# Kernel optimization log

Measured on AMD Instinct MI355X. Metric: run time of the kernel, lower is better.

## Reference

```python
import jax, jax.numpy as jnp
import numpy as np

N = 50000
E = 800000
F_IN = 128
H = 128
C = 16


def _balanced_conv(x, row, col, W, b, num_nodes):
    # x: [N, in] -> linear -> gather(row) * norm -> scatter-add(col) + bias
    x = x @ W  # [N, out]
    deg = jax.ops.segment_sum(jnp.ones(row.shape[0], x.dtype), col,
                              num_segments=num_nodes)  # includes self-loops -> deg >= 1
    dinv = deg ** -0.5
    norm = dinv[row] * dinv[col]  # [E+N]
    msg = norm[:, None] * x[row]  # gather + scale
    out = jax.ops.segment_sum(msg, col, num_segments=num_nodes)  # scatter-add
    return out + b


def setup_inputs() -> dict:
    key = jax.random.key(0)
    ks = jax.random.split(key, 12)
    x = jax.random.normal(ks[0], (N, F_IN), dtype=jnp.float32)
    edge_index = jax.random.randint(ks[1], (2, E), 0, N, dtype=jnp.int64)
    s = 1.0 / np.sqrt(F_IN)
    sh = 1.0 / np.sqrt(H)
    return {
        "x": x,
        "edge_index": edge_index,
        "importance": jnp.ones((F_IN,), jnp.float32),
        "W1": jax.random.uniform(ks[2], (F_IN, H), jnp.float32, -s, s),
        "b1": jnp.zeros((H,), jnp.float32),
        "W2": jax.random.uniform(ks[3], (H, H), jnp.float32, -sh, sh),
        "b2": jnp.zeros((H,), jnp.float32),
        "W3": jax.random.uniform(ks[4], (H, H), jnp.float32, -sh, sh),
        "b3": jnp.zeros((H,), jnp.float32),
        "lw1": jax.random.uniform(ks[5], (H, H), jnp.float32, -sh, sh),
        "lb1": jax.random.uniform(ks[6], (H,), jnp.float32, -sh, sh),
        "lw2": jax.random.uniform(ks[7], (H, C), jnp.float32, -sh, sh),
        "lb2": jax.random.uniform(ks[8], (C,), jnp.float32, -sh, sh),
    }


def reference(x, edge_index, importance, W1, b1, W2, b2, W3, b3, lw1, lb1, lw2, lb2):
    num_nodes = x.shape[0]
    # add self-loops (static shape: E + N)
    loops = jnp.arange(num_nodes, dtype=edge_index.dtype)
    row = jnp.concatenate([edge_index[0], loops])
    col = jnp.concatenate([edge_index[1], loops])

    gelu = lambda t: jax.nn.gelu(t, approximate=False)  # torch F.gelu default = erf

    h = x * importance  # FeatureImportance
    h = gelu(_balanced_conv(h, row, col, W1, b1, num_nodes))
    h = gelu(_balanced_conv(h, row, col, W2, b2, num_nodes))
    h = gelu(_balanced_conv(h, row, col, W3, b3, num_nodes))
    h = gelu(h @ lw1 + lb1)
    return h @ lw2 + lb2  # [N, C]
```

## Files before the change

### kernel.cpp

```cpp
#include <hip/hip_runtime.h>
#include <math.h>

#define NNODES 50000
#define NEDGES 800000
#define FDIM 128
#define NBUCKET 196
#define BCAP 6144
#define ABLK 261
#define EPWA 3072
#define MGRID 782

typedef unsigned short ushortT;
typedef unsigned int uintT;
typedef __attribute__((ext_vector_type(8))) short short8;
typedef __attribute__((ext_vector_type(4))) float floatx4;

__device__ __forceinline__ float gelu_erf(float x){
    return 0.5f * x * (1.0f + erff(x * 0.70710678118654752f));
}
__device__ __forceinline__ float bflo(uintT u){ return __uint_as_float(u << 16); }
__device__ __forceinline__ float bfhi(uintT u){ return __uint_as_float(u & 0xFFFF0000u); }
__device__ __forceinline__ ushortT f2bf(float f){
    uintT u = __float_as_uint(f);
    return (ushortT)((u + 0x7FFFu + ((u >> 16) & 1u)) >> 16);
}
__device__ __forceinline__ void split_bf16(float f, ushortT& hi, ushortT& lo){
    uintT u = __float_as_uint(f);
    hi = (ushortT)(u >> 16);
    float fhi = __uint_as_float(u & 0xFFFF0000u);
    lo = (ushortT)(__float_as_uint(f - fhi) >> 16);
}

__global__ void k_zero(int* __restrict__ gcur){
    if (threadIdx.x < NBUCKET) gcur[threadIdx.x] = 0;
}

__global__ __launch_bounds__(256) void k_bucketA(const int* __restrict__ ei,
                                                 int* __restrict__ gcur,
                                                 uintT* __restrict__ bucket){
    __shared__ int hist[NBUCKET];
    __shared__ int base[NBUCKET];
    int t = threadIdx.x;
    if (t < NBUCKET) hist[t] = 0;
    __syncthreads();
    int e0 = blockIdx.x * EPWA;
    int cr_c[12], cr_r[12];
    #pragma unroll
    for (int p = 0; p < 12; p++){
        int e = e0 + p*256 + t;
        if (e < NEDGES){
            cr_r[p] = ei[e];
            cr_c[p] = ei[NEDGES + e];
            atomicAdd(&hist[cr_c[p] >> 8], 1);
        } else cr_c[p] = -1;
    }
    __syncthreads();
    if (t < NBUCKET){
        base[t] = atomicAdd(&gcur[t], hist[t]);
        hist[t] = 0;
    }
    __syncthreads();
    #pragma unroll
    for (int p = 0; p < 12; p++){
        int c = cr_c[p];
        if (c >= 0){
            int b = c >> 8;
            int lp = atomicAdd(&hist[b], 1);
            bucket[(size_t)b*BCAP + base[b] + lp] = ((uintT)c << 16) | (uintT)cr_r[p];
        }
    }
}

__global__ __launch_bounds__(256) void k_bucketB(const int* __restrict__ gcur,
                                                 const uintT* __restrict__ bucket,
                                                 int* __restrict__ offs,
                                                 float* __restrict__ dinv,
                                                 ushortT* __restrict__ csr2){
    __shared__ int sm[256];
    __shared__ int hist[256];
    __shared__ int lcur[256];
    int b = blockIdx.x;
    int t = threadIdx.x;
    int n0 = b << 8;

    int gv = (t < NBUCKET) ? gcur[t] : 0;
    sm[t] = gv;
    __syncthreads();
    for (int off = 1; off < 256; off <<= 1){
        int tv = (t >= off) ? sm[t-off] : 0;
        __syncthreads();
        sm[t] += tv;
        __syncthreads();
    }
    __shared__ int bbase_s;
    if (t == b) bbase_s = sm[t] - gv;
    hist[t] = 0;
    __syncthreads();
    int bbase = bbase_s;
    int count = gcur[b];
    const uintT* src = bucket + (size_t)b*BCAP;

    for (int i = t; i < count; i += 256)
        atomicAdd(&hist[(src[i] >> 16) & 255], 1);
    __syncthreads();

    int v = hist[t];
    sm[t] = v;
    __syncthreads();
    for (int off = 1; off < 256; off <<= 1){
        int tv = (t >= off) ? sm[t-off] : 0;
        __syncthreads();
        sm[t] += tv;
        __syncthreads();
    }
    int excl = bbase + sm[t] - v;
    int node = n0 + t;
    if (node <= NNODES) offs[node] = excl;
    if (node < NNODES) dinv[node] = rsqrtf((float)(v + 1));
    if (b == NBUCKET-1 && t == 255) offs[NNODES] = NEDGES;
    lcur[t] = excl;
    __syncthreads();

    for (int i = t; i < count; i += 256){
        uintT e = src[i];
        int pos = atomicAdd(&lcur[(e >> 16) & 255], 1);
        csr2[pos] = (ushortT)(e & 0xFFFFu);
    }
}

__global__ __launch_bounds__(256) void k_packW(const float* __restrict__ Wa,
                                               const float* __restrict__ Wb,
                                               const float* __restrict__ Wc,
                                               const float* __restrict__ Wd,
                                               ushortT* __restrict__ Wp){
    int l = blockIdx.x;
    const float* W = (l==0) ? Wa : (l==1) ? Wb : (l==2) ? Wc : Wd;
    ushortT* hiP = Wp + (size_t)l*2*16384;
    ushortT* loP = hiP + 16384;
    for (int idx = threadIdx.x; idx < 16384; idx += 256){
        int k = idx >> 7, n = idx & 127;
        ushortT hi, lo;
        split_bf16(W[idx], hi, lo);
        int kc = k >> 5, quad = (k >> 3) & 3, j = k & 7;
        int nt = n >> 4, lane = (n & 15) + (quad << 4);
        int off = ((kc*8 + nt)*64 + lane)*8 + j;
        hiP[off] = hi;
        loP[off] = lo;
    }
}

template<int OUTMODE>
__global__ __launch_bounds__(256) void k_mfma(const float* __restrict__ A,
                                              const ushortT* __restrict__ Wp,
                                              const float* __restrict__ scale,
                                              const float* __restrict__ dinv,
                                              const float* __restrict__ bias,
                                              void* __restrict__ Yout){
    int t = threadIdx.x;
    int wave = t >> 6, lane = t & 63;
    int r = lane & 15, quad = lane >> 4;
    int m0 = blockIdx.x*64 + wave*16;
    int arow = m0 + r;
    if (arow >= NNODES) arow = NNODES - 1;
    const ushortT* WpLo = Wp + 16384;

    floatx4 acc[8];
    #pragma unroll
    for (int nt = 0; nt < 8; nt++) acc[nt] = (floatx4){0.f,0.f,0.f,0.f};

    #pragma unroll
    for (int kc = 0; kc < 4; kc++){
        int kb = kc*32 + quad*8;
        float4 a0 = *(const float4*)&A[(size_t)arow*FDIM + kb];
        float4 a1 = *(const float4*)&A[(size_t)arow*FDIM + kb + 4];
        if (scale){
            float4 s0 = *(const float4*)&scale[kb];
            float4 s1 = *(const float4*)&scale[kb + 4];
            a0.x*=s0.x; a0.y*=s0.y; a0.z*=s0.z; a0.w*=s0.w;
            a1.x*=s1.x; a1.y*=s1.y; a1.z*=s1.z; a1.w*=s1.w;
        }
        float av[8] = {a0.x, a0.y, a0.z, a0.w, a1.x, a1.y, a1.z, a1.w};
        short8 ahi, alo;
        #pragma unroll
        for (int e = 0; e < 8; e++){
            ushortT h, l;
            split_bf16(av[e], h, l);
            ahi[e] = (short)h;
            alo[e] = (short)l;
        }
        #pragma unroll
        for (int nt = 0; nt < 8; nt++){
            size_t boff = (size_t)(((kc*8 + nt)*64 + lane))*8;
            short8 bhi = *(const short8*)&Wp[boff];
            short8 blo = *(const short8*)&WpLo[boff];
            acc[nt] = __builtin_amdgcn_mfma_f32_16x16x32_bf16(ahi, bhi, acc[nt], 0, 0, 0);
            acc[nt] = __builtin_amdgcn_mfma_f32_16x16x32_bf16(alo, bhi, acc[nt], 0, 0, 0);
            acc[nt] = __builtin_amdgcn_mfma_f32_16x16x32_bf16(ahi, blo, acc[nt], 0, 0, 0);
        }
    }

    int orow0 = m0 + quad*4;
    if (OUTMODE == 1){
        float4 dv = *(const float4*)&dinv[orow0];
        float dva[4] = {dv.x, dv.y, dv.z, dv.w};
        ushortT* Yb = (ushortT*)Yout;
        #pragma unroll
        for (int nt = 0; nt < 8; nt++){
            int n = nt*16 + r;
            int chunk = n >> 5, o = n & 31;
            #pragma unroll
            for (int reg = 0; reg < 4; reg++){
                int orow = orow0 + reg;
                if (orow < NNODES){
                    float v = acc[nt][reg] * dva[reg];
                    Yb[((size_t)chunk*NNODES + orow)*32 + o] = f2bf(v);
                }
            }
        }
    } else {
        float* Yf = (float*)Yout;
        #pragma unroll
        for (int nt = 0; nt < 8; nt++){
            int n = nt*16 + r;
            float bv = bias[n];
            #pragma unroll
            for (int reg = 0; reg < 4; reg++){
                int orow = orow0 + reg;
                if (orow < NNODES){
                    Yf[(size_t)orow*FDIM + n] = gelu_erf(acc[nt][reg] + bv);
                }
            }
        }
    }
}

__global__ __launch_bounds__(256) void k_aggregate(const ushortT* __restrict__ Yt,
                                                   const float* __restrict__ dinv,
                                                   const int* __restrict__ offs,
                                                   const ushortT* __restrict__ csr2,
                                                   const float* __restrict__ bias,
                                                   float* __restrict__ Hout){
    int bid = blockIdx.x;
    int chunk = bid & 3;
    int node = (bid >> 2) * 16 + (threadIdx.x >> 4);
    int lane = threadIdx.x & 15;
    const uintT* Yc = (const uintT*)Yt + (size_t)chunk * NNODES * 16;

    uintT a0 = Yc[node*16 + lane];
    float2 acc;
    acc.x = bflo(a0);
    acc.y = bfhi(a0);
    int e0 = offs[node], e1 = offs[node+1];
    int e = e0;
    for (; e + 3 < e1; e += 4){
        int r0 = csr2[e+0];
        int r1 = csr2[e+1];
        int r2 = csr2[e+2];
        int r3 = csr2[e+3];
        uintT q0 = Yc[r0*16 + lane];
        uintT q1 = Yc[r1*16 + lane];
        uintT q2 = Yc[r2*16 + lane];
        uintT q3 = Yc[r3*16 + lane];
        acc.x += bflo(q0); acc.y += bfhi(q0);
        acc.x += bflo(q1); acc.y += bfhi(q1);
        acc.x += bflo(q2); acc.y += bfhi(q2);
        acc.x += bflo(q3); acc.y += bfhi(q3);
    }
    for (; e < e1; e++){
        int r = csr2[e];
        uintT q = Yc[r*16 + lane];
        acc.x += bflo(q); acc.y += bfhi(q);
    }
    float dc = dinv[node];
    float2 bv = ((const float2*)bias)[chunk*16 + lane];
    acc.x = gelu_erf(fmaf(dc, acc.x, bv.x));
    acc.y = gelu_erf(fmaf(dc, acc.y, bv.y));
    float* dst = &Hout[(size_t)node*FDIM + chunk*32 + lane*2];
    __builtin_nontemporal_store(acc.x, dst);
    __builtin_nontemporal_store(acc.y, dst+1);
}

__global__ __launch_bounds__(256) void k_gemm16(const float* __restrict__ A,
                                                const float* __restrict__ W,
                                                const float* __restrict__ bias,
                                                float* __restrict__ out){
    __shared__ float Hs[16][132];
    __shared__ float Ws2[128][16];
    int row0 = blockIdx.x * 16;
    int t = threadIdx.x;
    #pragma unroll
    for (int p=0;p<8;p++){
        int lin = p*256 + t;
        int r = lin >> 7, c = lin & 127;
        Hs[r][c] = A[(row0+r)*FDIM + c];
    }
    #pragma unroll
    for (int p=0;p<8;p++){
        int lin = p*256 + t;
        Ws2[lin>>4][lin&15] = W[lin];
    }
    __syncthreads();
    int il = t >> 4, j = t & 15;
    float acc = bias[j];
    #pragma unroll
    for (int k=0;k<FDIM;k++) acc = fmaf(Hs[il][k], Ws2[k][j], acc);
    out[(row0+il)*16 + j] = acc;
}

extern "C" void kernel_launch(void* const* d_in, const int* in_sizes, int n_in,
                              void* d_out, int out_size, void* d_ws, size_t ws_size,
                              hipStream_t stream) {
    const float* x    = (const float*)d_in[0];
    const int*   ei   = (const int*)d_in[1];
    const float* imp  = (const float*)d_in[2];
    const float* W1   = (const float*)d_in[3];
    const float* b1   = (const float*)d_in[4];
    const float* W2   = (const float*)d_in[5];
    const float* b2   = (const float*)d_in[6];
    const float* W3   = (const float*)d_in[7];
    const float* b3   = (const float*)d_in[8];
    const float* lw1  = (const float*)d_in[9];
    const float* lb1  = (const float*)d_in[10];
    const float* lw2  = (const float*)d_in[11];
    const float* lb2  = (const float*)d_in[12];
    float* out = (float*)d_out;

    int*   offs   = (int*)d_ws;
    int*   gcur   = (int*)d_ws + 50048;
    float* dinv   = (float*)d_ws + 50304;
    ushortT* csr2 = (ushortT*)((int*)d_ws + 100480);
    uintT* bucket = (uintT*)((int*)d_ws + 500480);
    ushortT* Wp   = (ushortT*)((int*)d_ws + 1704704);
    ushortT* bufYt= (ushortT*)((int*)d_ws + 1770240);
    float* bufY   = (float*)d_ws + 1770240;
    float* bufH   = (float*)d_ws + 8170240;

    dim3 B(256);
    k_packW  <<<4, B, 0, stream>>>(W1, W2, W3, lw1, Wp);
    k_zero   <<<1, B, 0, stream>>>(gcur);
    k_bucketA<<<ABLK, B, 0, stream>>>(ei, gcur, bucket);
    k_bucketB<<<NBUCKET, B, 0, stream>>>(gcur, bucket, offs, dinv, csr2);

    k_mfma<1><<<MGRID, B, 0, stream>>>(x,    Wp + 0*32768, imp,     dinv, nullptr, (void*)bufYt);
    k_aggregate<<<(NNODES/16)*4, B, 0, stream>>>(bufYt, dinv, offs, csr2, b1, bufH);
    k_mfma<1><<<MGRID, B, 0, stream>>>(bufH, Wp + 1*32768, nullptr, dinv, nullptr, (void*)bufYt);
    k_aggregate<<<(NNODES/16)*4, B, 0, stream>>>(bufYt, dinv, offs, csr2, b2, bufH);
    k_mfma<1><<<MGRID, B, 0, stream>>>(bufH, Wp + 2*32768, nullptr, dinv, nullptr, (void*)bufYt);
    k_aggregate<<<(NNODES/16)*4, B, 0, stream>>>(bufYt, dinv, offs, csr2, b3, bufH);

    k_mfma<0><<<MGRID, B, 0, stream>>>(bufH, Wp + 3*32768, nullptr, nullptr, lb1, (void*)bufY);
    k_gemm16<<<NNODES/16, B, 0, stream>>>(bufY, lw2, lb2, out);
}
```

Before: 360.7 us.

## Stage GEMM A tile through LDS, nontemporal bf16 stores, unroll gather by eight

The MFMA GEMM kernel now loads its 64-row A tile into shared memory with coalesced float4 loads, applying the feature scale there, before the per-lane fragment reads. Previously each lane read its row with strided global loads. Its bf16 output stores become nontemporal. The aggregation loop is unrolled from 4 to 8 neighbours with a 2-wide tail, putting more independent gathers in flight at the cost of extra registers and about 33KB of LDS per GEMM block.

```diff
diff --git a/kernel.cpp b/kernel.cpp
--- a/kernel.cpp
+++ b/kernel.cpp
@@ -156,29 +156,40 @@
                                               const float* __restrict__ dinv,
                                               const float* __restrict__ bias,
                                               void* __restrict__ Yout){
+    __shared__ float As[64*132];
     int t = threadIdx.x;
     int wave = t >> 6, lane = t & 63;
     int r = lane & 15, quad = lane >> 4;
-    int m0 = blockIdx.x*64 + wave*16;
-    int arow = m0 + r;
-    if (arow >= NNODES) arow = NNODES - 1;
+    int row0 = blockIdx.x*64;
+    int m0 = row0 + wave*16;
     const ushortT* WpLo = Wp + 16384;
 
+    #pragma unroll
+    for (int p = 0; p < 8; p++){
+        int idx = p*256 + t;
+        int rr = idx >> 5;
+        int c4 = idx & 31;
+        int gr = row0 + rr;
+        float4 v = make_float4(0.f,0.f,0.f,0.f);
+        if (gr < NNODES) v = *(const float4*)&A[(size_t)gr*FDIM + c4*4];
+        if (scale){
+            float4 s = *(const float4*)&scale[c4*4];
+            v.x*=s.x; v.y*=s.y; v.z*=s.z; v.w*=s.w;
+        }
+        *(float4*)&As[rr*132 + c4*4] = v;
+    }
+    __syncthreads();
+
     floatx4 acc[8];
     #pragma unroll
     for (int nt = 0; nt < 8; nt++) acc[nt] = (floatx4){0.f,0.f,0.f,0.f};
 
+    int arl = wave*16 + r;
     #pragma unroll
     for (int kc = 0; kc < 4; kc++){
         int kb = kc*32 + quad*8;
-        float4 a0 = *(const float4*)&A[(size_t)arow*FDIM + kb];
-        float4 a1 = *(const float4*)&A[(size_t)arow*FDIM + kb + 4];
-        if (scale){
-            float4 s0 = *(const float4*)&scale[kb];
-            float4 s1 = *(const float4*)&scale[kb + 4];
-            a0.x*=s0.x; a0.y*=s0.y; a0.z*=s0.z; a0.w*=s0.w;
-            a1.x*=s1.x; a1.y*=s1.y; a1.z*=s1.z; a1.w*=s1.w;
-        }
+        float4 a0 = *(const float4*)&As[arl*132 + kb];
+        float4 a1 = *(const float4*)&As[arl*132 + kb + 4];
         float av[8] = {a0.x, a0.y, a0.z, a0.w, a1.x, a1.y, a1.z, a1.w};
         short8 ahi, alo;
         #pragma unroll
@@ -213,7 +224,8 @@
                 int orow = orow0 + reg;
                 if (orow < NNODES){
                     float v = acc[nt][reg] * dva[reg];
-                    Yb[((size_t)chunk*NNODES + orow)*32 + o] = f2bf(v);
+                    __builtin_nontemporal_store(f2bf(v),
+                        &Yb[((size_t)chunk*NNODES + orow)*32 + o]);
                 }
             }
         }
@@ -252,23 +264,41 @@
     acc.y = bfhi(a0);
     int e0 = offs[node], e1 = offs[node+1];
     int e = e0;
-    for (; e + 3 < e1; e += 4){
+    for (; e + 7 < e1; e += 8){
         int r0 = csr2[e+0];
         int r1 = csr2[e+1];
         int r2 = csr2[e+2];
         int r3 = csr2[e+3];
+        int r4 = csr2[e+4];
+        int r5 = csr2[e+5];
+        int r6 = csr2[e+6];
+        int r7 = csr2[e+7];
         uintT q0 = Yc[r0*16 + lane];
         uintT q1 = Yc[r1*16 + lane];
         uintT q2 = Yc[r2*16 + lane];
         uintT q3 = Yc[r3*16 + lane];
+        uintT q4 = Yc[r4*16 + lane];
+        uintT q5 = Yc[r5*16 + lane];
+        uintT q6 = Yc[r6*16 + lane];
+        uintT q7 = Yc[r7*16 + lane];
         acc.x += bflo(q0); acc.y += bfhi(q0);
         acc.x += bflo(q1); acc.y += bfhi(q1);
         acc.x += bflo(q2); acc.y += bfhi(q2);
         acc.x += bflo(q3); acc.y += bfhi(q3);
-    }
-    for (; e < e1; e++){
-        int r = csr2[e];
-        uintT q = Yc[r*16 + lane];
+        acc.x += bflo(q4); acc.y += bfhi(q4);
+        acc.x += bflo(q5); acc.y += bfhi(q5);
+        acc.x += bflo(q6); acc.y += bfhi(q6);
+        acc.x += bflo(q7); acc.y += bfhi(q7);
+    }
+    for (; e + 1 < e1; e += 2){
+        int r0 = csr2[e], r1 = csr2[e+1];
+        uintT q0 = Yc[r0*16 + lane];
+        uintT q1 = Yc[r1*16 + lane];
+        acc.x += bflo(q0); acc.y += bfhi(q0);
+        acc.x += bflo(q1); acc.y += bfhi(q1);
+    }
+    if (e < e1){
+        uintT q = Yc[csr2[e]*16 + lane];
         acc.x += bflo(q); acc.y += bfhi(q);
     }
     float dc = dinv[node];
```

Measured after the change: 346.7 us. 3.9% less time.
